# Kernel optimization log

Hardware: AMD Instinct MI355X
Metric: run time of the kernel (lower is better)

## Reference

```python
import jax, jax.numpy as jnp
import numpy as np

B, S, E, H = 2, 2048, 1024, 16
DH = E // H  # 64
EPS = 1e-5


def layer_norm(x, g, b):
    mu = jnp.mean(x, axis=-1, keepdims=True)
    var = jnp.mean(jnp.square(x - mu), axis=-1, keepdims=True)
    return (x - mu) * jax.lax.rsqrt(var + EPS) * g + b


def setup_inputs() -> dict:
    key = jax.random.key(0)
    ks = jax.random.split(key, 12)
    s = lambda fan_in: 1.0 / np.sqrt(fan_in)
    return {
        "x": jax.random.normal(ks[0], (B, S, E), dtype=jnp.float32),
        "ln1_g": jnp.ones((E,), jnp.float32),
        "ln1_b": jnp.zeros((E,), jnp.float32),
        # per-head projections, batched over head axis: [H, E, DH]
        "Wq": jax.random.uniform(ks[1], (H, E, DH), jnp.float32, -s(E), s(E)),
        "Wk": jax.random.uniform(ks[2], (H, E, DH), jnp.float32, -s(E), s(E)),
        "Wv": jax.random.uniform(ks[3], (H, E, DH), jnp.float32, -s(E), s(E)),
        "Wo": jax.random.uniform(ks[4], (H * DH, E), jnp.float32, -s(H * DH), s(H * DH)),
        "bo": jax.random.uniform(ks[5], (E,), jnp.float32, -s(H * DH), s(H * DH)),
        "ln2_g": jnp.ones((E,), jnp.float32),
        "ln2_b": jnp.zeros((E,), jnp.float32),
        "W1": jax.random.uniform(ks[6], (E, 4 * E), jnp.float32, -s(E), s(E)),
        "b1": jax.random.uniform(ks[7], (4 * E,), jnp.float32, -s(E), s(E)),
        "W2": jax.random.uniform(ks[8], (4 * E, E), jnp.float32, -s(4 * E), s(4 * E)),
        "b2": jax.random.uniform(ks[9], (E,), jnp.float32, -s(4 * E), s(4 * E)),
    }


def reference(x, ln1_g, ln1_b, Wq, Wk, Wv, Wo, bo, ln2_g, ln2_b, W1, b1, W2, b2):
    b, s, e = x.shape
    # --- multi-head attention (pre-LN) ---
    h = layer_norm(x, ln1_g, ln1_b)
    q = jnp.einsum("bse,hed->bhsd", h, Wq)
    k = jnp.einsum("bse,hed->bhsd", h, Wk)
    v = jnp.einsum("bse,hed->bhsd", h, Wv)
    # NOTE: original scales by channel**-0.5 (embed_size), not head_size
    scores = jnp.einsum("bhsd,bhtd->bhst", q, k) * (e ** -0.5)
    causal = jnp.tril(jnp.ones((s, s), dtype=bool))
    scores = jnp.where(causal, scores, -jnp.inf)
    attn = jax.nn.softmax(scores, axis=-1)  # dropout is identity in eval
    out = jnp.einsum("bhst,bhtd->bhsd", attn, v)
    out = out.transpose(0, 2, 1, 3).reshape(b, s, -1)  # concat heads: [B,S,H*DH]
    x = x + out @ Wo + bo
    # --- feed-forward (pre-LN) ---
    h2 = layer_norm(x, ln2_g, ln2_b)
    ff = jax.nn.relu(h2 @ W1 + b1) @ W2 + b2
    return x + ff
```

## Files before the change

### kernel.cpp

```cpp
#include <hip/hip_runtime.h>


typedef __bf16 bf16_t;
typedef __attribute__((ext_vector_type(8))) __bf16 bf16x8;
typedef __attribute__((ext_vector_type(4))) __bf16 bf16x4;
typedef __attribute__((ext_vector_type(4))) float f32x4;

#define B_DIM 2
#define S_DIM 2048
#define E_DIM 1024
#define H_DIM 16
#define DH_DIM 64

#define GLD16(gp, lp) __builtin_amdgcn_global_load_lds( \
    (const __attribute__((address_space(1))) void*)(gp), \
    (__attribute__((address_space(3))) void*)(lp), 16, 0, 0)

#define Q_SCALE 0.0450842120f

__global__ __launch_bounds__(256) void ln_kernel(
    const float* __restrict__ x, const float* __restrict__ g,
    const float* __restrict__ bv, bf16_t* __restrict__ out)
{
  const int row = blockIdx.x;
  const int t = threadIdx.x;
  const float* xr = x + (size_t)row * E_DIM;
  float4 v = *(const float4*)&xr[t * 4];
  float s  = v.x + v.y + v.z + v.w;
  float s2 = v.x*v.x + v.y*v.y + v.z*v.z + v.w*v.w;
#pragma unroll
  for (int m = 1; m < 64; m <<= 1) {
    s  += __shfl_xor(s,  m, 64);
    s2 += __shfl_xor(s2, m, 64);
  }
  __shared__ float red[8];
  const int wid = t >> 6, lane = t & 63;
  if (lane == 0) { red[wid] = s; red[4 + wid] = s2; }
  __syncthreads();
  s  = red[0] + red[1] + red[2] + red[3];
  s2 = red[4] + red[5] + red[6] + red[7];
  const float mu  = s * (1.f / E_DIM);
  const float var = s2 * (1.f / E_DIM) - mu * mu;
  const float rs  = rsqrtf(var + 1e-5f);
  float4 gg = *(const float4*)&g[t * 4];
  float4 bb = *(const float4*)&bv[t * 4];
  bf16x4 o;
  o[0] = (bf16_t)((v.x - mu) * rs * gg.x + bb.x);
  o[1] = (bf16_t)((v.y - mu) * rs * gg.y + bb.y);
  o[2] = (bf16_t)((v.z - mu) * rs * gg.z + bb.z);
  o[3] = (bf16_t)((v.w - mu) * rs * gg.w + bb.w);
  *(bf16x4*)&out[(size_t)row * E_DIM + t * 4] = o;
}

__global__ __launch_bounds__(256) void reduce2_ln(
    const bf16_t* __restrict__ p0, const bf16_t* __restrict__ p1,
    const float* __restrict__ bo, const float* __restrict__ x,
    const float* __restrict__ g, const float* __restrict__ bv,
    float* __restrict__ xmid, bf16_t* __restrict__ h2)
{
  const int row = blockIdx.x;
  const int t = threadIdx.x;
  const size_t off = (size_t)row * E_DIM + t * 4;
  bf16x4 a = *(const bf16x4*)&p0[off];
  bf16x4 b4 = *(const bf16x4*)&p1[off];
  float4 xr = *(const float4*)&x[off];
  float4 bo4 = *(const float4*)&bo[t * 4];
  float4 v;
  v.x = (float)a[0] + (float)b4[0] + xr.x + bo4.x;
  v.y = (float)a[1] + (float)b4[1] + xr.y + bo4.y;
  v.z = (float)a[2] + (float)b4[2] + xr.z + bo4.z;
  v.w = (float)a[3] + (float)b4[3] + xr.w + bo4.w;
  *(float4*)&xmid[off] = v;
  float s  = v.x + v.y + v.z + v.w;
  float s2 = v.x*v.x + v.y*v.y + v.z*v.z + v.w*v.w;
#pragma unroll
  for (int m = 1; m < 64; m <<= 1) {
    s  += __shfl_xor(s,  m, 64);
    s2 += __shfl_xor(s2, m, 64);
  }
  __shared__ float red[8];
  const int wid = t >> 6, lane = t & 63;
  if (lane == 0) { red[wid] = s; red[4 + wid] = s2; }
  __syncthreads();
  s  = red[0] + red[1] + red[2] + red[3];
  s2 = red[4] + red[5] + red[6] + red[7];
  const float mu  = s * (1.f / E_DIM);
  const float var = s2 * (1.f / E_DIM) - mu * mu;
  const float rs  = rsqrtf(var + 1e-5f);
  float4 gg = *(const float4*)&g[t * 4];
  float4 bb = *(const float4*)&bv[t * 4];
  bf16x4 o;
  o[0] = (bf16_t)((v.x - mu) * rs * gg.x + bb.x);
  o[1] = (bf16_t)((v.y - mu) * rs * gg.y + bb.y);
  o[2] = (bf16_t)((v.z - mu) * rs * gg.z + bb.z);
  o[3] = (bf16_t)((v.w - mu) * rs * gg.w + bb.w);
  *(bf16x4*)&h2[off] = o;
}

__global__ __launch_bounds__(256) void reduce4(
    const bf16_t* __restrict__ p0, const bf16_t* __restrict__ p1,
    const bf16_t* __restrict__ p2, const bf16_t* __restrict__ p3,
    const float* __restrict__ b2, const float* __restrict__ xm,
    float* __restrict__ out)
{
  const int row = blockIdx.x;
  const int t = threadIdx.x;
  const size_t off = (size_t)row * E_DIM + t * 4;
  bf16x4 a0 = *(const bf16x4*)&p0[off];
  bf16x4 a1 = *(const bf16x4*)&p1[off];
  bf16x4 a2 = *(const bf16x4*)&p2[off];
  bf16x4 a3 = *(const bf16x4*)&p3[off];
  float4 xr = *(const float4*)&xm[off];
  float4 bb = *(const float4*)&b2[t * 4];
  float4 o;
  o.x = (float)a0[0] + (float)a1[0] + (float)a2[0] + (float)a3[0] + xr.x + bb.x;
  o.y = (float)a0[1] + (float)a1[1] + (float)a2[1] + (float)a3[1] + xr.y + bb.y;
  o.z = (float)a0[2] + (float)a1[2] + (float)a2[2] + (float)a3[2] + xr.z + bb.z;
  o.w = (float)a0[3] + (float)a1[3] + (float)a2[3] + (float)a3[3] + xr.w + bb.w;
  *(float4*)&out[off] = o;
}

__global__ __launch_bounds__(256) void transpose_cast(
    const float* __restrict__ src, bf16_t* __restrict__ dst, int R, int C)
{
  __shared__ float tile[64][65];
  const int c0 = blockIdx.x * 64, r0 = blockIdx.y * 64;
  const int t = threadIdx.x;
  const int rr = t >> 2;
#pragma unroll
  for (int u = 0; u < 4; u++) {
    const int cc = (t & 3) * 4 + u * 16;
    float4 f = *(const float4*)&src[(size_t)(r0 + rr) * C + c0 + cc];
    tile[rr][cc + 0] = f.x; tile[rr][cc + 1] = f.y;
    tile[rr][cc + 2] = f.z; tile[rr][cc + 3] = f.w;
  }
  __syncthreads();
  const int oc = t >> 2;
#pragma unroll
  for (int u = 0; u < 4; u++) {
    const int orr = (t & 3) * 4 + u * 16;
    bf16x4 w;
    w[0] = (bf16_t)tile[orr + 0][oc];
    w[1] = (bf16_t)tile[orr + 1][oc];
    w[2] = (bf16_t)tile[orr + 2][oc];
    w[3] = (bf16_t)tile[orr + 3][oc];
    *(bf16x4*)&dst[(size_t)(c0 + oc) * R + r0 + orr] = w;
  }
}

__global__ __launch_bounds__(256) void qkv_transpose(
    const float* __restrict__ Wq, const float* __restrict__ Wk,
    const float* __restrict__ Wv, bf16_t* __restrict__ dstT)
{
  const int m = blockIdx.y >> 4, h = blockIdx.y & 15;
  const float* src = (m == 0 ? Wq : (m == 1 ? Wk : Wv)) + (size_t)h * E_DIM * DH_DIM;
  const int e0 = blockIdx.x * 64;
  __shared__ float tile[64][65];
  const int t = threadIdx.x;
  const int rr = t >> 2;
#pragma unroll
  for (int u = 0; u < 4; u++) {
    const int cc = (t & 3) * 4 + u * 16;
    float4 f = *(const float4*)&src[(size_t)(e0 + rr) * DH_DIM + cc];
    tile[rr][cc + 0] = f.x; tile[rr][cc + 1] = f.y;
    tile[rr][cc + 2] = f.z; tile[rr][cc + 3] = f.w;
  }
  __syncthreads();
  const int oc = t >> 2;
  const size_t drow = (size_t)(m * 1024 + h * 64 + oc) * E_DIM;
#pragma unroll
  for (int u = 0; u < 4; u++) {
    const int orr = (t & 3) * 4 + u * 16;
    bf16x4 w;
    w[0] = (bf16_t)tile[orr + 0][oc];
    w[1] = (bf16_t)tile[orr + 1][oc];
    w[2] = (bf16_t)tile[orr + 2][oc];
    w[3] = (bf16_t)tile[orr + 3][oc];
    *(bf16x4*)&dstT[drow + e0 + orr] = w;
  }
}

constexpr int EPI_QKV = 0, EPI_BIAS_RELU = 2, EPI_PART_F32 = 3, EPI_PART_B16 = 4;

template <int EPI>
__global__ __launch_bounds__(256) void gemm128_kernel(
    const bf16_t* __restrict__ A, const bf16_t* __restrict__ Bt,
    int M, int N, int Kst, int Klen,
    const float* __restrict__ bias,
    float* __restrict__ outF, bf16_t* __restrict__ outB,
    bf16_t* __restrict__ qo, bf16_t* __restrict__ ko, bf16_t* __restrict__ vo)
{
  __shared__ bf16_t As[2][128 * 32];
  __shared__ bf16_t Bs[2][128 * 32];
  const int gx = gridDim.x;
  const int nwg = gx * gridDim.y;
  int id = blockIdx.y * gx + blockIdx.x;
  id = (id & 7) * (nwg >> 3) + (id >> 3);
  const int m0 = (id % gx) * 128, n0 = (id / gx) * 128;
  const int sp = blockIdx.z;
  A  += (size_t)sp * Klen;
  Bt += (size_t)sp * Klen;

  const int tid = threadIdx.x, lane = tid & 63, wid = tid >> 6;
  const int wr = wid >> 1, wc = wid & 1;
  const int lr = lane & 15, lg = lane >> 4;
  const int halfr = lr >> 1;
  const int sl16 = (((lr & 1) * 4 + lg) ^ halfr) * 16;
  const int baseA = (wr * 32 + halfr) * 128 + sl16;
  const int baseB = (wc * 32 + halfr) * 128 + sl16;

  auto stage = [&](int kt, int buf) {
#pragma unroll
    for (int p = 0; p < 2; p++) {
      const int L = p * 256 + tid;
      const int row2 = L >> 3;
      const int s = (L & 7) ^ (row2 & 7);
      const int r = row2 * 2 + (s >> 2);
      const int u = s & 3;
      char* lb = (char*)&As[buf][0] + (size_t)(p * 256 + wid * 64) * 16;
      char* lbB = (char*)&Bs[buf][0] + (size_t)(p * 256 + wid * 64) * 16;
      GLD16(A  + (size_t)(m0 + r) * Kst + kt * 32 + u * 8, lb);
      GLD16(Bt + (size_t)(n0 + r) * Kst + kt * 32 + u * 8, lbB);
    }
  };

  const f32x4 z4 = {0.f, 0.f, 0.f, 0.f};
  f32x4 acc[4][4];
#pragma unroll
  for (int i = 0; i < 4; i++)
#pragma unroll
    for (int j = 0; j < 4; j++) acc[i][j] = z4;

  const int NT = Klen / 32;
  stage(0, 0);
  for (int T = 0; T < NT; ++T) {
    const int b = T & 1;
    asm volatile("s_waitcnt vmcnt(0)" ::: "memory");
    __builtin_amdgcn_s_barrier();
    if (T + 1 < NT) stage(T + 1, b ^ 1);
    __builtin_amdgcn_sched_barrier(0);

    bf16x8 af[4], bfr[4];
#pragma unroll
    for (int j = 0; j < 4; j++)
      bfr[j] = *(const bf16x8*)((const char*)&Bs[b][0] + baseB + j * 1024);
#pragma unroll
    for (int i = 0; i < 4; i++)
      af[i] = *(const bf16x8*)((const char*)&As[b][0] + baseA + i * 1024);
    __builtin_amdgcn_s_setprio(1);
#pragma unroll
    for (int i = 0; i < 4; i++)
#pragma unroll
      for (int j = 0; j < 4; j++)
        acc[i][j] = __builtin_amdgcn_mfma_f32_16x16x32_bf16(af[i], bfr[j], acc[i][j], 0, 0, 0);
    __builtin_amdgcn_s_setprio(0);
  }

#pragma unroll
  for (int i = 0; i < 4; i++) {
#pragma unroll
    for (int j = 0; j < 4; j++) {
#pragma unroll
      for (int r = 0; r < 4; r++) {
        const int m = m0 + wr * 64 + i * 16 + lg * 4 + r;
        const int n = n0 + wc * 64 + j * 16 + lr;
        const float val = acc[i][j][r];
        if constexpr (EPI == EPI_QKV) {
          const int tsel = n >> 10, h = (n >> 6) & 15, d = n & 63;
          const int b_ = m >> 11, s_ = m & 2047;
          if (tsel == 0)
            qo[((size_t)((b_ * H_DIM + h) * S_DIM + s_)) * DH_DIM + d] = (bf16_t)(val * Q_SCALE);
          else if (tsel == 1)
            ko[((size_t)((b_ * H_DIM + h) * S_DIM + s_)) * DH_DIM + d] = (bf16_t)val;
          else
            vo[((size_t)((b_ * H_DIM + h) * DH_DIM + d)) * S_DIM + s_] = (bf16_t)val;
        } else if constexpr (EPI == EPI_BIAS_RELU) {
          const float u = val + bias[n];
          outB[(size_t)m * N + n] = (bf16_t)(u > 0.f ? u : 0.f);
        } else if constexpr (EPI == EPI_PART_F32) {
          outF[(size_t)sp * M * N + (size_t)m * N + n] = val;
        } else {
          bf16_t* o = sp == 0 ? outB : sp == 1 ? qo : sp == 2 ? ko : vo;
          o[(size_t)m * N + n] = (bf16_t)val;
        }
      }
    }
  }
}

template <int EPI>
__global__ __launch_bounds__(512) void gemm256_kernel(
    const bf16_t* __restrict__ A, const bf16_t* __restrict__ Bt,
    int M, int N, int Kst, int Klen,
    const float* __restrict__ bias,
    float* __restrict__ outF, bf16_t* __restrict__ outB,
    bf16_t* __restrict__ qo, bf16_t* __restrict__ ko, bf16_t* __restrict__ vo)
{
  __shared__ bf16_t As[2][256 * 64];
  __shared__ bf16_t Bs[2][256 * 64];
  const int gx = gridDim.x;
  const int nwg = gx * gridDim.y;
  int id = blockIdx.y * gx + blockIdx.x;
  id = (id & 7) * (nwg >> 3) + (id >> 3);
  const int m0 = (id % gx) * 256, n0 = (id / gx) * 256;
  const int sp = blockIdx.z;
  A  += (size_t)sp * Klen;
  Bt += (size_t)sp * Klen;

  const int tid = threadIdx.x, lane = tid & 63, wid = tid >> 6;
  const int wm = wid >> 2, wn = wid & 3;
  const int lr = lane & 15, lg = lane >> 4;
  const int l7 = lr & 7;
  const int sl[2] = { (lg ^ l7) * 16, ((4 | lg) ^ l7) * 16 };
  const int rbA = (wm * 128 + lr) * 128;
  const int rbB = (wn * 64 + lr) * 128;

  auto stage = [&](int kt, int buf) {
#pragma unroll
    for (int q = 0; q < 4; q++) {
      const int L = q * 512 + tid;
      const int row = L >> 3;
      const int u = (L & 7) ^ (row & 7);
      char* la = (char*)&As[buf][0] + (size_t)(q * 512 + wid * 64) * 16;
      char* lb = (char*)&Bs[buf][0] + (size_t)(q * 512 + wid * 64) * 16;
      GLD16(A  + (size_t)(m0 + row) * Kst + kt * 64 + u * 8, la);
      GLD16(Bt + (size_t)(n0 + row) * Kst + kt * 64 + u * 8, lb);
    }
  };

  const f32x4 z4 = {0.f, 0.f, 0.f, 0.f};
  f32x4 acc[8][4];
#pragma unroll
  for (int i = 0; i < 8; i++)
#pragma unroll
    for (int j = 0; j < 4; j++) acc[i][j] = z4;

  const int NT = Klen / 64;
  stage(0, 0);
  for (int T = 0; T < NT; ++T) {
    const int b = T & 1;
    asm volatile("s_waitcnt vmcnt(0)" ::: "memory");
    __builtin_amdgcn_s_barrier();
    if (T + 1 < NT) stage(T + 1, b ^ 1);
    __builtin_amdgcn_sched_barrier(0);

    bf16x8 bfr[2][4];
#pragma unroll
    for (int kk = 0; kk < 2; kk++)
#pragma unroll
      for (int j = 0; j < 4; j++)
        bfr[kk][j] = *(const bf16x8*)((const char*)&Bs[b][0] + rbB + j * 2048 + sl[kk]);
    __builtin_amdgcn_s_setprio(1);
#pragma unroll
    for (int i = 0; i < 8; i++) {
#pragma unroll
      for (int kk = 0; kk < 2; kk++) {
        bf16x8 af = *(const bf16x8*)((const char*)&As[b][0] + rbA + i * 2048 + sl[kk]);
#pragma unroll
        for (int j = 0; j < 4; j++)
          acc[i][j] = __builtin_amdgcn_mfma_f32_16x16x32_bf16(af, bfr[kk][j], acc[i][j], 0, 0, 0);
      }
    }
    __builtin_amdgcn_s_setprio(0);
  }

#pragma unroll
  for (int i = 0; i < 8; i++) {
#pragma unroll
    for (int j = 0; j < 4; j++) {
#pragma unroll
      for (int r = 0; r < 4; r++) {
        const int m = m0 + wm * 128 + i * 16 + lg * 4 + r;
        const int n = n0 + wn * 64 + j * 16 + lr;
        const float val = acc[i][j][r];
        if constexpr (EPI == EPI_BIAS_RELU) {
          const float u = val + bias[n];
          outB[(size_t)m * N + n] = (bf16_t)(u > 0.f ? u : 0.f);
        } else if constexpr (EPI == EPI_PART_F32) {
          outF[(size_t)sp * M * N + (size_t)m * N + n] = val;
        } else if constexpr (EPI == EPI_PART_B16) {
          bf16_t* o = sp == 0 ? outB : sp == 1 ? qo : sp == 2 ? ko : vo;
          o[(size_t)m * N + n] = (bf16_t)val;
        }
      }
    }
  }
}

__global__ __launch_bounds__(256) void attn_kernel(
    const bf16_t* __restrict__ Q, const bf16_t* __restrict__ K,
    const bf16_t* __restrict__ Vt, bf16_t* __restrict__ O,
    bf16_t* __restrict__ Opart, float* __restrict__ mpart, float* __restrict__ lpart)
{
  __shared__ bf16_t Ks[2][64 * 64];
  __shared__ bf16_t Vs[2][64 * 64];
  __shared__ bf16_t Ps[4][2][16 * 64];

  const int nwg = 51 * gridDim.y;
  int id = blockIdx.y * 51 + blockIdx.x;
  id = (id & 7) * (nwg >> 3) + (id >> 3);
  const int bx = id % 51, bh = id / 51;

  int g = 0;
  while (3 * (g + 1) * (g + 2) / 2 <= bx) g++;
  const int rr_ = bx - 3 * g * (g + 1) / 2;
  const int q2 = 3 * g + rr_ / (g + 1);
  const int sp = rr_ % (g + 1);
  const int ns = g + 1;
  const int n2 = 2 * q2 + 2;
  const int lo = 6 * sp;
  const int hi = (6 * sp + 6 < n2) ? 6 * sp + 6 : n2;

  const int tid = threadIdx.x;
  const int wid = tid >> 6, lane = tid & 63;
  const int lr = lane & 15, lg = lane >> 4;
  const int q0w = q2 * 128 + wid * 32;

  const bf16_t* Qp = Q  + (size_t)bh * S_DIM * DH_DIM;
  const bf16_t* Kp = K  + (size_t)bh * S_DIM * DH_DIM;
  const bf16_t* Vp = Vt + (size_t)bh * DH_DIM * S_DIM;

  bf16x8 bq0[2], bq1[2];
#pragma unroll
  for (int c = 0; c < 2; c++) {
    bq0[c] = *(const bf16x8*)&Qp[(size_t)(q0w + lr) * DH_DIM + c * 32 + lg * 8];
    bq1[c] = *(const bf16x8*)&Qp[(size_t)(q0w + 16 + lr) * DH_DIM + c * 32 + lg * 8];
  }

  const f32x4 z4 = {0.f, 0.f, 0.f, 0.f};
  f32x4 Ot0[4], Ot1[4];
#pragma unroll
  for (int dt = 0; dt < 4; dt++) { Ot0[dt] = z4; Ot1[dt] = z4; }
  float mrow0 = -1e30f, lrow0 = 0.f;
  float mrow1 = -1e30f, lrow1 = 0.f;

  const int ktr = wid * 8 + (lane >> 3);
  const int ksc = lane & 7;

  auto stageKV = [&](int t0, int buf) {
#pragma unroll
    for (int p = 0; p < 2; p++) {
      const int tr = p * 32 + ktr;
      GLD16(Kp + (size_t)(t0 + tr) * DH_DIM + (ksc ^ (tr & 7)) * 8,
            &Ks[buf][(p * 32 + wid * 8) * 64]);
      GLD16(Vp + (size_t)tr * S_DIM + t0 + (ksc ^ (tr & 7)) * 8,
            &Vs[buf][(p * 32 + wid * 8) * 64]);
    }
  };

  stageKV(lo * 64, 0);

  for (int tc = lo; tc < hi; ++tc) {
    const int cur = (tc - lo) & 1;
    __syncthreads();
    if (tc + 1 < hi) stageKV((tc + 1) * 64, cur ^ 1);

    const int t0 = tc * 64;
    f32x4 s0[4], s1[4];
    __builtin_amdgcn_s_setprio(1);
#pragma unroll
    for (int j = 0; j < 4; j++) {
      f32x4 a = z4, b = z4;
      const int t = j * 16 + lr;
#pragma unroll
      for (int c = 0; c < 2; c++) {
        const int kbyte = t * 128 + (((c * 4 + lg) * 16) ^ ((t & 7) << 4));
        bf16x8 ak = *(const bf16x8*)((const char*)&Ks[cur][0] + kbyte);
        a = __builtin_amdgcn_mfma_f32_16x16x32_bf16(ak, bq0[c], a, 0, 0, 0);
        b = __builtin_amdgcn_mfma_f32_16x16x32_bf16(ak, bq1[c], b, 0, 0, 0);
      }
      s0[j] = a; s1[j] = b;
    }
    __builtin_amdgcn_s_setprio(0);
    if (tc >= 2 * q2) {
#pragma unroll
      for (int j = 0; j < 4; j++)
#pragma unroll
        for (int r = 0; r < 4; r++) {
          const int tg = t0 + j * 16 + lg * 4 + r;
          if (tg > q0w + lr)      s0[j][r] = -1e30f;
          if (tg > q0w + 16 + lr) s1[j][r] = -1e30f;
        }
    }
    {
      float mj[4];
#pragma unroll
      for (int j = 0; j < 4; j++)
        mj[j] = fmaxf(fmaxf(s0[j][0], s0[j][1]), fmaxf(s0[j][2], s0[j][3]));
      float tmax = fmaxf(fmaxf(mj[0], mj[1]), fmaxf(mj[2], mj[3]));
      tmax = fmaxf(tmax, __shfl_xor(tmax, 16, 64));
      tmax = fmaxf(tmax, __shfl_xor(tmax, 32, 64));
      if (!__all(tmax <= mrow0 + 8.f)) {
        const float mnew = fmaxf(mrow0, tmax);
        const float fsc = __builtin_exp2f(mrow0 - mnew);
        mrow0 = mnew; lrow0 *= fsc;
#pragma unroll
        for (int dt = 0; dt < 4; dt++)
#pragma unroll
          for (int r = 0; r < 4; r++) Ot0[dt][r] *= fsc;
      }
      float sj[4];
#pragma unroll
      for (int j = 0; j < 4; j++) {
#pragma unroll
        for (int r = 0; r < 4; r++) s0[j][r] = __builtin_exp2f(s0[j][r] - mrow0);
        sj[j] = (s0[j][0] + s0[j][1]) + (s0[j][2] + s0[j][3]);
      }
      float tsum = (sj[0] + sj[1]) + (sj[2] + sj[3]);
      tsum += __shfl_xor(tsum, 16, 64);
      tsum += __shfl_xor(tsum, 32, 64);
      lrow0 += tsum;
#pragma unroll
      for (int j = 0; j < 4; j++) {
        bf16x4 w;
#pragma unroll
        for (int r = 0; r < 4; r++) w[r] = (bf16_t)s0[j][r];
        const int pbyte = lr * 128 + ((j * 32 + lg * 8) ^ ((lr & 7) << 4));
        *(bf16x4*)((char*)&Ps[wid][0][0] + pbyte) = w;
      }
    }
    {
      float mj[4];
#pragma unroll
      for (int j = 0; j < 4; j++)
        mj[j] = fmaxf(fmaxf(s1[j][0], s1[j][1]), fmaxf(s1[j][2], s1[j][3]));
      float tmax = fmaxf(fmaxf(mj[0], mj[1]), fmaxf(mj[2], mj[3]));
      tmax = fmaxf(tmax, __shfl_xor(tmax, 16, 64));
      tmax = fmaxf(tmax, __shfl_xor(tmax, 32, 64));
      if (!__all(tmax <= mrow1 + 8.f)) {
        const float mnew = fmaxf(mrow1, tmax);
        const float fsc = __builtin_exp2f(mrow1 - mnew);
        mrow1 = mnew; lrow1 *= fsc;
#pragma unroll
        for (int dt = 0; dt < 4; dt++)
#pragma unroll
          for (int r = 0; r < 4; r++) Ot1[dt][r] *= fsc;
      }
      float sj[4];
#pragma unroll
      for (int j = 0; j < 4; j++) {
#pragma unroll
        for (int r = 0; r < 4; r++) s1[j][r] = __builtin_exp2f(s1[j][r] - mrow1);
        sj[j] = (s1[j][0] + s1[j][1]) + (s1[j][2] + s1[j][3]);
      }
      float tsum = (sj[0] + sj[1]) + (sj[2] + sj[3]);
      tsum += __shfl_xor(tsum, 16, 64);
      tsum += __shfl_xor(tsum, 32, 64);
      lrow1 += tsum;
#pragma unroll
      for (int j = 0; j < 4; j++) {
        bf16x4 w;
#pragma unroll
        for (int r = 0; r < 4; r++) w[r] = (bf16_t)s1[j][r];
        const int pbyte = lr * 128 + ((j * 32 + lg * 8) ^ ((lr & 7) << 4));
        *(bf16x4*)((char*)&Ps[wid][1][0] + pbyte) = w;
      }
    }

    __builtin_amdgcn_s_setprio(1);
#pragma unroll
    for (int c = 0; c < 2; c++) {
      const int abyte = lr * 128 + ((c * 64 + lg * 16) ^ ((lr & 7) << 4));
      bf16x8 pa0 = *(const bf16x8*)((const char*)&Ps[wid][0][0] + abyte);
      bf16x8 pa1 = *(const bf16x8*)((const char*)&Ps[wid][1][0] + abyte);
#pragma unroll
      for (int dt = 0; dt < 4; dt++) {
        const int d = dt * 16 + lr;
        const int vbyte = d * 128 + (((c * 4 + lg) * 16) ^ ((d & 7) << 4));
        bf16x8 bv = *(const bf16x8*)((const char*)&Vs[cur][0] + vbyte);
        Ot0[dt] = __builtin_amdgcn_mfma_f32_16x16x32_bf16(bv, pa0, Ot0[dt], 0, 0, 0);
        Ot1[dt] = __builtin_amdgcn_mfma_f32_16x16x32_bf16(bv, pa1, Ot1[dt], 0, 0, 0);
      }
    }
    __builtin_amdgcn_s_setprio(0);
  }

  if (ns == 1) {
    const int b = bh >> 4, h = bh & 15;
    {
      const float linv = 1.f / lrow0;
      const size_t base = ((size_t)(b * S_DIM + q0w + lr)) * E_DIM + h * DH_DIM;
#pragma unroll
      for (int dt = 0; dt < 4; dt++) {
        bf16x4 w;
#pragma unroll
        for (int r = 0; r < 4; r++) w[r] = (bf16_t)(Ot0[dt][r] * linv);
        *(bf16x4*)&O[base + dt * 16 + lg * 4] = w;
      }
    }
    {
      const float linv = 1.f / lrow1;
      const size_t base = ((size_t)(b * S_DIM + q0w + 16 + lr)) * E_DIM + h * DH_DIM;
#pragma unroll
      for (int dt = 0; dt < 4; dt++) {
        bf16x4 w;
#pragma unroll
        for (int r = 0; r < 4; r++) w[r] = (bf16_t)(Ot1[dt][r] * linv);
        *(bf16x4*)&O[base + dt * 16 + lg * 4] = w;
      }
    }
  } else {
    const int psl = bh * 48 + (bx - 3);
    bf16_t* Ob = Opart + (size_t)psl * 128 * 64;
    const int row0 = wid * 32 + lr, row1 = row0 + 16;
#pragma unroll
    for (int dt = 0; dt < 4; dt++) {
      bf16x4 w0, w1;
#pragma unroll
      for (int r = 0; r < 4; r++) { w0[r] = (bf16_t)Ot0[dt][r]; w1[r] = (bf16_t)Ot1[dt][r]; }
      *(bf16x4*)&Ob[row0 * 64 + dt * 16 + lg * 4] = w0;
      *(bf16x4*)&Ob[row1 * 64 + dt * 16 + lg * 4] = w1;
    }
    if (lg == 0) {
      mpart[psl * 128 + row0] = mrow0;
      lpart[psl * 128 + row0] = lrow0;
      mpart[psl * 128 + row1] = mrow1;
      lpart[psl * 128 + row1] = lrow1;
    }
  }
}

__global__ __launch_bounds__(256) void attn_combine(
    const bf16_t* __restrict__ Opart, const float* __restrict__ mpart,
    const float* __restrict__ lpart, bf16_t* __restrict__ O)
{
  const int q2 = 3 + (blockIdx.x >> 1);
  const int half = blockIdx.x & 1;
  const int bh = blockIdx.y;
  const int g = q2 / 3, ns = g + 1;
  const int sbase = 3 * g * (g + 1) / 2 + (q2 - 3 * g) * (g + 1) - 3;
  const int psl0 = bh * 48 + sbase;
  const int tid = threadIdx.x;
  const int q = tid >> 2, d0 = (tid & 3) * 16;
  const int row = half * 64 + q;

  float M = -1e30f;
  for (int s = 0; s < ns; s++) M = fmaxf(M, mpart[(psl0 + s) * 128 + row]);
  float L = 0.f;
  float acc[16];
#pragma unroll
  for (int j = 0; j < 16; j++) acc[j] = 0.f;
  for (int s = 0; s < ns; s++) {
    const float w = __builtin_exp2f(mpart[(psl0 + s) * 128 + row] - M);
    L += w * lpart[(psl0 + s) * 128 + row];
    const bf16_t* Ob = Opart + ((size_t)(psl0 + s) * 128 + row) * 64 + d0;
    bf16x8 o0 = *(const bf16x8*)Ob;
    bf16x8 o1 = *(const bf16x8*)(Ob + 8);
#pragma unroll
    for (int j = 0; j < 8; j++) { acc[j] += w * (float)o0[j]; acc[8 + j] += w * (float)o1[j]; }
  }
  const float inv = 1.f / L;
  const int b = bh >> 4, h = bh & 15;
  const int srow = q2 * 128 + row;
  bf16_t* out = O + ((size_t)(b * S_DIM + srow)) * E_DIM + h * DH_DIM + d0;
  bf16x8 w0, w1;
#pragma unroll
  for (int j = 0; j < 8; j++) { w0[j] = (bf16_t)(acc[j] * inv); w1[j] = (bf16_t)(acc[8 + j] * inv); }
  *(bf16x8*)out = w0;
  *(bf16x8*)(out + 8) = w1;
}

extern "C" void kernel_launch(void* const* d_in, const int* in_sizes, int n_in,
                              void* d_out, int out_size, void* d_ws, size_t ws_size,
                              hipStream_t stream)
{
  const float* x    = (const float*)d_in[0];
  const float* ln1g = (const float*)d_in[1];
  const float* ln1b = (const float*)d_in[2];
  const float* Wq   = (const float*)d_in[3];
  const float* Wk   = (const float*)d_in[4];
  const float* Wv   = (const float*)d_in[5];
  const float* Wo   = (const float*)d_in[6];
  const float* bo   = (const float*)d_in[7];
  const float* ln2g = (const float*)d_in[8];
  const float* ln2b = (const float*)d_in[9];
  const float* W1   = (const float*)d_in[10];
  const float* b1   = (const float*)d_in[11];
  const float* W2   = (const float*)d_in[12];
  const float* b2   = (const float*)d_in[13];

  char* ws = (char*)d_ws;
  bf16_t* WqkvT = (bf16_t*)(ws + 0);
  bf16_t* WoT   = (bf16_t*)(ws + 6291456);
  bf16_t* W1T   = (bf16_t*)(ws + 8388608);
  bf16_t* W2T   = (bf16_t*)(ws + 16777216);
  bf16_t* h1    = (bf16_t*)(ws + 25165824);
  bf16_t* qb    = (bf16_t*)(ws + 33554432);
  bf16_t* kb    = (bf16_t*)(ws + 41943040);
  bf16_t* vb    = (bf16_t*)(ws + 50331648);
  bf16_t* attnb = (bf16_t*)(ws + 58720256);
  float*  xmid  = (float* )(ws + 67108864);
  bf16_t* h2    = (bf16_t*)(ws + 83886080);
  bf16_t* ff1   = (bf16_t*)(ws + 25165824);
  bf16_t* Opart = (bf16_t*)(ws + 67108864);
  float*  mpart = (float* )(ws + 25165824);
  float*  lpart = (float* )(ws + 25952256);
  bf16_t* po0   = (bf16_t*)(ws + 25165824);
  bf16_t* po1   = (bf16_t*)(ws + 33554432);
  bf16_t* pf0   = (bf16_t*)(ws + 0);
  bf16_t* pf1   = (bf16_t*)(ws + 8388608);
  bf16_t* pf2   = (bf16_t*)(ws + 58720256);
  bf16_t* pf3   = (bf16_t*)(ws + 83886080);

  qkv_transpose<<<dim3(16, 48), 256, 0, stream>>>(Wq, Wk, Wv, WqkvT);
  transpose_cast<<<dim3(16, 16), 256, 0, stream>>>(Wo, WoT, 1024, 1024);
  transpose_cast<<<dim3(64, 16), 256, 0, stream>>>(W1, W1T, 1024, 4096);
  transpose_cast<<<dim3(16, 64), 256, 0, stream>>>(W2, W2T, 4096, 1024);

  ln_kernel<<<4096, 256, 0, stream>>>(x, ln1g, ln1b, h1);
  gemm128_kernel<EPI_QKV><<<dim3(32, 24, 1), 256, 0, stream>>>(
      h1, WqkvT, 4096, 3072, 1024, 1024, nullptr,
      nullptr, nullptr, qb, kb, vb);
  attn_kernel<<<dim3(51, 32), 256, 0, stream>>>(qb, kb, vb, attnb, Opart, mpart, lpart);
  attn_combine<<<dim3(26, 32), 256, 0, stream>>>(Opart, mpart, lpart, attnb);
  gemm128_kernel<EPI_PART_B16><<<dim3(32, 8, 2), 256, 0, stream>>>(
      attnb, WoT, 4096, 1024, 1024, 512, nullptr,
      nullptr, po0, po1, nullptr, nullptr);
  reduce2_ln<<<4096, 256, 0, stream>>>(po0, po1, bo, x, ln2g, ln2b, xmid, h2);
  gemm256_kernel<EPI_BIAS_RELU><<<dim3(16, 16, 1), 512, 0, stream>>>(
      h2, W1T, 4096, 4096, 1024, 1024, b1,
      nullptr, ff1, nullptr, nullptr, nullptr);
  gemm256_kernel<EPI_PART_B16><<<dim3(16, 4, 4), 512, 0, stream>>>(
      ff1, W2T, 4096, 1024, 4096, 1024, nullptr,
      nullptr, pf0, pf1, pf2, pf3);
  reduce4<<<4096, 256, 0, stream>>>(pf0, pf1, pf2, pf3, b2, xmid, (float*)d_out);

  (void)in_sizes; (void)n_in; (void)out_size; (void)ws_size;
}
```

Measured before the change: 259.2 us.

## Deepen gemm128 K-tile to 64 and map workgroups to per-XCD rectangular regions

The 128x128 GEMM now stages 64-wide K slices instead of 32, using a new XOR-swizzled LDS layout. That halves the number of barrier and wait iterations and issues twice the MFMAs per step, at the cost of doubling LDS use to 64KB. Both GEMM kernels replace the old XCD round-robin remap with an explicit mapping that gives each XCD a compact RM x RN block of output tiles, so that operand tiles are reused in that XCD's L2. The region sizes are passed per launch.

```diff
diff --git a/kernel.cpp b/kernel.cpp
--- a/kernel.cpp
+++ b/kernel.cpp
@@ -182,21 +182,24 @@
 
 constexpr int EPI_QKV = 0, EPI_BIAS_RELU = 2, EPI_PART_F32 = 3, EPI_PART_B16 = 4;
 
+
 template <int EPI>
 __global__ __launch_bounds__(256) void gemm128_kernel(
     const bf16_t* __restrict__ A, const bf16_t* __restrict__ Bt,
-    int M, int N, int Kst, int Klen,
+    int M, int N, int Kst, int Klen, int RM, int RN,
     const float* __restrict__ bias,
     float* __restrict__ outF, bf16_t* __restrict__ outB,
     bf16_t* __restrict__ qo, bf16_t* __restrict__ ko, bf16_t* __restrict__ vo)
 {
-  __shared__ bf16_t As[2][128 * 32];
-  __shared__ bf16_t Bs[2][128 * 32];
+  __shared__ bf16_t As[2][128 * 64];
+  __shared__ bf16_t Bs[2][128 * 64];
   const int gx = gridDim.x;
-  const int nwg = gx * gridDim.y;
-  int id = blockIdx.y * gx + blockIdx.x;
-  id = (id & 7) * (nwg >> 3) + (id >> 3);
-  const int m0 = (id % gx) * 128, n0 = (id / gx) * 128;
+  const int lin = blockIdx.y * gx + blockIdx.x;
+  const int xcd = lin & 7, kb = lin >> 3;
+  const int nregx = gx / RM;
+  const int rx = xcd % nregx, ry = xcd / nregx;
+  const int m0 = (rx * RM + kb % RM) * 128;
+  const int n0 = (ry * RN + kb / RM) * 128;
   const int sp = blockIdx.z;
   A  += (size_t)sp * Klen;
   Bt += (size_t)sp * Klen;
@@ -204,23 +207,21 @@
   const int tid = threadIdx.x, lane = tid & 63, wid = tid >> 6;
   const int wr = wid >> 1, wc = wid & 1;
   const int lr = lane & 15, lg = lane >> 4;
-  const int halfr = lr >> 1;
-  const int sl16 = (((lr & 1) * 4 + lg) ^ halfr) * 16;
-  const int baseA = (wr * 32 + halfr) * 128 + sl16;
-  const int baseB = (wc * 32 + halfr) * 128 + sl16;
+  const int l7 = lr & 7;
+  const int sl[2] = { (lg ^ l7) * 16, ((4 | lg) ^ l7) * 16 };
+  const int rbA = (wr * 64 + lr) * 128;
+  const int rbB = (wc * 64 + lr) * 128;
 
   auto stage = [&](int kt, int buf) {
 #pragma unroll
-    for (int p = 0; p < 2; p++) {
-      const int L = p * 256 + tid;
-      const int row2 = L >> 3;
-      const int s = (L & 7) ^ (row2 & 7);
-      const int r = row2 * 2 + (s >> 2);
-      const int u = s & 3;
-      char* lb = (char*)&As[buf][0] + (size_t)(p * 256 + wid * 64) * 16;
-      char* lbB = (char*)&Bs[buf][0] + (size_t)(p * 256 + wid * 64) * 16;
-      GLD16(A  + (size_t)(m0 + r) * Kst + kt * 32 + u * 8, lb);
-      GLD16(Bt + (size_t)(n0 + r) * Kst + kt * 32 + u * 8, lbB);
+    for (int q = 0; q < 4; q++) {
+      const int L = q * 256 + tid;
+      const int row = L >> 3;
+      const int u = (L & 7) ^ (row & 7);
+      char* la = (char*)&As[buf][0] + (size_t)(q * 256 + wid * 64) * 16;
+      char* lb = (char*)&Bs[buf][0] + (size_t)(q * 256 + wid * 64) * 16;
+      GLD16(A  + (size_t)(m0 + row) * Kst + kt * 64 + u * 8, la);
+      GLD16(Bt + (size_t)(n0 + row) * Kst + kt * 64 + u * 8, lb);
     }
   };
 
@@ -231,7 +232,7 @@
 #pragma unroll
     for (int j = 0; j < 4; j++) acc[i][j] = z4;
 
-  const int NT = Klen / 32;
+  const int NT = Klen / 64;
   stage(0, 0);
   for (int T = 0; T < NT; ++T) {
     const int b = T & 1;
@@ -240,19 +241,23 @@
     if (T + 1 < NT) stage(T + 1, b ^ 1);
     __builtin_amdgcn_sched_barrier(0);
 
-    bf16x8 af[4], bfr[4];
-#pragma unroll
-    for (int j = 0; j < 4; j++)
-      bfr[j] = *(const bf16x8*)((const char*)&Bs[b][0] + baseB + j * 1024);
-#pragma unroll
-    for (int i = 0; i < 4; i++)
-      af[i] = *(const bf16x8*)((const char*)&As[b][0] + baseA + i * 1024);
+    bf16x8 bfr[2][4];
+#pragma unroll
+    for (int kk = 0; kk < 2; kk++)
+#pragma unroll
+      for (int j = 0; j < 4; j++)
+        bfr[kk][j] = *(const bf16x8*)((const char*)&Bs[b][0] + rbB + j * 2048 + sl[kk]);
     __builtin_amdgcn_s_setprio(1);
 #pragma unroll
-    for (int i = 0; i < 4; i++)
-#pragma unroll
-      for (int j = 0; j < 4; j++)
-        acc[i][j] = __builtin_amdgcn_mfma_f32_16x16x32_bf16(af[i], bfr[j], acc[i][j], 0, 0, 0);
+    for (int i = 0; i < 4; i++) {
+#pragma unroll
+      for (int kk = 0; kk < 2; kk++) {
+        bf16x8 af = *(const bf16x8*)((const char*)&As[b][0] + rbA + i * 2048 + sl[kk]);
+#pragma unroll
+        for (int j = 0; j < 4; j++)
+          acc[i][j] = __builtin_amdgcn_mfma_f32_16x16x32_bf16(af, bfr[kk][j], acc[i][j], 0, 0, 0);
+      }
+    }
     __builtin_amdgcn_s_setprio(0);
   }
 
@@ -291,7 +296,7 @@
 template <int EPI>
 __global__ __launch_bounds__(512) void gemm256_kernel(
     const bf16_t* __restrict__ A, const bf16_t* __restrict__ Bt,
-    int M, int N, int Kst, int Klen,
+    int M, int N, int Kst, int Klen, int RM, int RN,
     const float* __restrict__ bias,
     float* __restrict__ outF, bf16_t* __restrict__ outB,
     bf16_t* __restrict__ qo, bf16_t* __restrict__ ko, bf16_t* __restrict__ vo)
@@ -299,10 +304,12 @@
   __shared__ bf16_t As[2][256 * 64];
   __shared__ bf16_t Bs[2][256 * 64];
   const int gx = gridDim.x;
-  const int nwg = gx * gridDim.y;
-  int id = blockIdx.y * gx + blockIdx.x;
-  id = (id & 7) * (nwg >> 3) + (id >> 3);
-  const int m0 = (id % gx) * 256, n0 = (id / gx) * 256;
+  const int lin = blockIdx.y * gx + blockIdx.x;
+  const int xcd = lin & 7, kb = lin >> 3;
+  const int nregx = gx / RM;
+  const int rx = xcd % nregx, ry = xcd / nregx;
+  const int m0 = (rx * RM + kb % RM) * 256;
+  const int n0 = (ry * RN + kb / RM) * 256;
   const int sp = blockIdx.z;
   A  += (size_t)sp * Klen;
   Bt += (size_t)sp * Klen;
@@ -709,19 +716,19 @@
 
   ln_kernel<<<4096, 256, 0, stream>>>(x, ln1g, ln1b, h1);
   gemm128_kernel<EPI_QKV><<<dim3(32, 24, 1), 256, 0, stream>>>(
-      h1, WqkvT, 4096, 3072, 1024, 1024, nullptr,
+      h1, WqkvT, 4096, 3072, 1024, 1024, 8, 12, nullptr,
       nullptr, nullptr, qb, kb, vb);
   attn_kernel<<<dim3(51, 32), 256, 0, stream>>>(qb, kb, vb, attnb, Opart, mpart, lpart);
   attn_combine<<<dim3(26, 32), 256, 0, stream>>>(Opart, mpart, lpart, attnb);
   gemm128_kernel<EPI_PART_B16><<<dim3(32, 8, 2), 256, 0, stream>>>(
-      attnb, WoT, 4096, 1024, 1024, 512, nullptr,
+      attnb, WoT, 4096, 1024, 1024, 512, 8, 4, nullptr,
       nullptr, po0, po1, nullptr, nullptr);
   reduce2_ln<<<4096, 256, 0, stream>>>(po0, po1, bo, x, ln2g, ln2b, xmid, h2);
   gemm256_kernel<EPI_BIAS_RELU><<<dim3(16, 16, 1), 512, 0, stream>>>(
-      h2, W1T, 4096, 4096, 1024, 1024, b1,
+      h2, W1T, 4096, 4096, 1024, 1024, 8, 4, b1,
       nullptr, ff1, nullptr, nullptr, nullptr);
   gemm256_kernel<EPI_PART_B16><<<dim3(16, 4, 4), 512, 0, stream>>>(
-      ff1, W2T, 4096, 1024, 4096, 1024, nullptr,
+      ff1, W2T, 4096, 1024, 4096, 1024, 4, 2, nullptr,
       nullptr, pf0, pf1, pf2, pf3);
   reduce4<<<4096, 256, 0, stream>>>(pf0, pf1, pf2, pf3, b2, xmid, (float*)d_out);
 
```

Measured after the change: 251.7 us. 2.9% less time.
